# Optimization experiments

Hardware: AMD Instinct MI355X
Metric: run time of the kernel (lower is better)

The kernel has to match this reference:

```python
import jax, jax.numpy as jnp
import numpy as np

B, S, D_MODEL, N_HEADS, MAX_LEN = 2, 1024, 1024, 16, 1024
D_K = D_MODEL // N_HEADS


def setup_inputs() -> dict:
    key = jax.random.key(0)
    ks = jax.random.split(key, 8)
    w_std = 1.0 / np.sqrt(D_MODEL)  # ~ torch Linear default scale
    inp = {
        "query": jax.random.normal(ks[0], (B, S, D_MODEL), jnp.float32),
        "key": jax.random.normal(ks[1], (B, S, D_MODEL), jnp.float32),
        "value": jax.random.normal(ks[2], (B, S, D_MODEL), jnp.float32),
        "Wq": jax.random.normal(ks[3], (D_MODEL, D_MODEL), jnp.float32) * w_std,
        "Wk": jax.random.normal(ks[4], (D_MODEL, D_MODEL), jnp.float32) * w_std,
        "Wv": jax.random.normal(ks[5], (D_MODEL, D_MODEL), jnp.float32) * w_std,
        "Wo": jax.random.normal(ks[6], (D_MODEL, D_MODEL), jnp.float32) * w_std,
        "bq": jnp.zeros((D_MODEL,), jnp.float32),
        "bk": jnp.zeros((D_MODEL,), jnp.float32),
        "bv": jnp.zeros((D_MODEL,), jnp.float32),
        "bo": jnp.zeros((D_MODEL,), jnp.float32),
        "Er": jax.random.normal(ks[7], (2 * MAX_LEN - 1, D_K), jnp.float32) * 0.02,
    }
    return inp


def _rel_positions(q_len, k_len, max_len):
    pos = jnp.arange(q_len)[:, None] - jnp.arange(k_len)[None, :]
    pos = jnp.clip(pos, -max_len + 1, max_len - 1)
    return pos + max_len - 1  # [q_len, k_len] indices into Er


def reference(query, key, value, Wq, Wk, Wv, Wo, bq, bk, bv, bo, Er):
    b, q_len, d_model = query.shape
    k_len = key.shape[1]
    d_k = Er.shape[-1]
    h = d_model // d_k
    scale = 1.0 / np.sqrt(d_k)

    def proj(x, W, bias):  # torch Linear: x @ W.T + b, then split heads -> [b,h,s,d_k]
        y = x @ W.T + bias
        return y.reshape(b, -1, h, d_k).transpose(0, 2, 1, 3)

    q = proj(query, Wq, bq)
    k = proj(key, Wk, bk)
    v = proj(value, Wv, bv)

    positions = _rel_positions(q_len, k_len, MAX_LEN)  # [q,k]
    # QEr[b,h,q,k] = sum_d q[b,h,q,d] * Er[positions[q,k], d]
    # computed as a full contraction against Er then a gather on the relative axis
    qe_all = jnp.einsum('bhqd,rd->bhqr', q, Er)  # [b,h,q,2*max_len-1]
    qer = jnp.take_along_axis(qe_all, positions[None, None, :, :], axis=-1)  # [b,h,q,k]

    qk = jnp.einsum('bhqd,bhkd->bhqk', q, k)
    scores = (qk + qer) * scale
    p_attn = jax.nn.softmax(scores, axis=-1)  # dropout=0.0 (eval)
    out = jnp.einsum('bhqk,bhkd->bhqd', p_attn, v)

    out = out.transpose(0, 2, 1, 3).reshape(b, q_len, h * d_k)
    return out @ Wo.T + bo
```

## Files before the change

### kernel.cpp

```cpp
#include <hip/hip_runtime.h>
#include <hip/hip_bf16.h>
#include <cstdint>
#include <cstddef>

typedef __attribute__((ext_vector_type(8))) short bf16x8;
typedef __attribute__((ext_vector_type(4))) float f32x4;
typedef unsigned short u16;
typedef unsigned int u32;

#define DEV static __device__ __forceinline__

constexpr int Sc = 1024, DMc = 1024, Hc = 16, DKc = 64;

DEV u16 f2bf(float f) {
  u32 u = __float_as_uint(f);
  return (u16)((u + 0x7FFFu + ((u >> 16) & 1u)) >> 16);
}
DEV float bf2f(u16 h) { return __uint_as_float(((u32)h) << 16); }

#define GLDS16(g, l)                                                        \
  __builtin_amdgcn_global_load_lds(                                         \
      (const __attribute__((address_space(1))) void*)(g),                   \
      (__attribute__((address_space(3))) void*)(l), 16, 0, 0)

struct CvtJob { const float* in; u16* out; int nchunk; int rsh; int nreal; };
struct CvtArgs { CvtJob j[8]; };

__global__ __launch_bounds__(256) void cvt_kernel(CvtArgs a) {
  CvtJob job = a.j[blockIdx.y];
  int ci = (int)(blockIdx.x * 256 + threadIdx.x);
  if (ci >= job.nchunk) return;
  bf16x8 o = {};
  if (ci < job.nreal) {
    const float* src = job.in + (size_t)ci * 8;
    float4 v0 = *(const float4*)src;
    float4 v1 = *(const float4*)(src + 4);
    o[0] = (short)f2bf(v0.x); o[1] = (short)f2bf(v0.y);
    o[2] = (short)f2bf(v0.z); o[3] = (short)f2bf(v0.w);
    o[4] = (short)f2bf(v1.x); o[5] = (short)f2bf(v1.y);
    o[6] = (short)f2bf(v1.z); o[7] = (short)f2bf(v1.w);
  }
  int row = ci >> job.rsh;
  int co = (ci & ~7) | ((ci & 7) ^ (row & 7));
  *(bf16x8*)(job.out + (size_t)co * 8) = o;
}

struct GemmJob { const u16* A; const u16* W; const float* bias; void* out; const float* aux; };
struct GemmArgs { GemmJob p[3]; };

template<int BM, int BN, int MODE>
__global__ __launch_bounds__(256, 2) void gemm_bt(GemmArgs G) {
  constexpr int MI = BM / 32, NI = BN / 32;
  __shared__ __align__(16) u16 sA[2][BM * 64];
  __shared__ __align__(16) u16 sB[2][BN * 64];
  const int tid = threadIdx.x, lane = tid & 63, w = tid >> 6;
  const int cl = lane & 15, rg = lane >> 4;
  const int srow = lane >> 3, schk = lane & 7;
  int z, m0, n0;
  if (MODE == 0) {
    int id = blockIdx.x;
    if (id < 512) {
      z = id >> 8;
      int r = id & 255, xcd = r & 7, t = r >> 3;
      m0 = (xcd * 4 + (t & 3)) * 64;
      n0 = (t >> 2) * 128;
    } else {
      z = 2;
      int r = id - 512, xcd = r & 7, t = r >> 3;
      n0 = (xcd * 2 + (t & 1)) * 128;
      m0 = (t >> 1) * 64;
    }
  } else {
    z = 0;
    int id = blockIdx.x, xcd = id & 7, t = id >> 3;
    m0 = (xcd * 4 + (t & 3)) * 64;
    n0 = (t >> 2) * 64;
  }
  GemmJob P = G.p[z];
  constexpr int K = 1024;
  const int wm = (w >> 1) * (BM / 2), wn = (w & 1) * (BN / 2);
  f32x4 acc[MI][NI] = {};

  bf16x8 ma[2][2];
  float  ml[2][2];

  auto stage = [&](int kt, int b) {
    if (MODE == 0) {
      const u16* Ab = P.A + (size_t)m0 * K + kt * 64;
      #pragma unroll
      for (int i = 0; i < BM / 32; ++i)
        GLDS16(Ab + (size_t)(i * 32 + w * 8 + srow) * K + schk * 8, &sA[b][(i * 32 + w * 8) * 64]);
    } else {
      #pragma unroll
      for (int i = 0; i < 2; ++i) {
        int ch = i * 256 + tid, row = ch >> 3, c = ch & 7;
        int rgl = m0 + row, bb = rgl >> 10, s = rgl & 1023;
        const u16* o0 = P.A + ((size_t)(bb * 16 + kt) * 1024 + s) * 64 + c * 8;
        ma[i][0] = *(const bf16x8*)o0;
        ma[i][1] = *(const bf16x8*)(o0 + (size_t)32 * 1024 * 64);
        ml[i][0] = P.aux[(size_t)(bb * 16 + kt) * 1024 + s];
        ml[i][1] = P.aux[(size_t)(32 + bb * 16 + kt) * 1024 + s];
      }
    }
    const u16* Wb = P.W + (size_t)n0 * K + kt * 64;
    #pragma unroll
    for (int i = 0; i < BN / 32; ++i)
      GLDS16(Wb + (size_t)(i * 32 + w * 8 + srow) * K + schk * 8, &sB[b][(i * 32 + w * 8) * 64]);
  };

  auto commit = [&](int b) {
    #pragma unroll
    for (int i = 0; i < 2; ++i) {
      int ch = i * 256 + tid, row = ch >> 3, c = ch & 7;
      float rinv = 1.0f / (ml[i][0] + ml[i][1]);
      bf16x8 v8;
      #pragma unroll
      for (int e = 0; e < 8; ++e)
        v8[e] = (short)f2bf((bf2f((u16)ma[i][0][e]) + bf2f((u16)ma[i][1][e])) * rinv);
      *(bf16x8*)(sA[b] + row * 64 + (c ^ (row & 7)) * 8) = v8;
    }
  };

  stage(0, 0);
  if (MODE == 1) commit(0);
  for (int kt = 0; kt < 16; ++kt) {
    __syncthreads();
    const int b = kt & 1;
    if (kt < 15) stage(kt + 1, b ^ 1);
    const u16* A_ = sA[b];
    const u16* B_ = sB[b];
    #pragma unroll
    for (int kk = 0; kk < 2; ++kk) {
      bf16x8 af[MI], bfr[NI];
      #pragma unroll
      for (int mi = 0; mi < MI; ++mi) {
        int row = wm + mi * 16 + cl;
        af[mi] = *(const bf16x8*)(A_ + row * 64 + ((kk * 4 + rg) ^ (row & 7)) * 8);
      }
      #pragma unroll
      for (int ni = 0; ni < NI; ++ni) {
        int row = wn + ni * 16 + cl;
        bfr[ni] = *(const bf16x8*)(B_ + row * 64 + ((kk * 4 + rg) ^ (row & 7)) * 8);
      }
      #pragma unroll
      for (int mi = 0; mi < MI; ++mi)
        #pragma unroll
        for (int ni = 0; ni < NI; ++ni)
          acc[mi][ni] = __builtin_amdgcn_mfma_f32_16x16x32_bf16(af[mi], bfr[ni], acc[mi][ni], 0, 0, 0);
    }
    if (MODE == 1 && kt < 15) commit(b ^ 1);
  }
  #pragma unroll
  for (int mi = 0; mi < MI; ++mi) {
    #pragma unroll
    for (int ni = 0; ni < NI; ++ni) {
      #pragma unroll
      for (int j = 0; j < 4; ++j) {
        int m = m0 + wm + mi * 16 + rg * 4 + j;
        int n = n0 + wn + ni * 16 + cl;
        if (MODE == 1) {
          ((float*)P.out)[(size_t)m * DMc + n] = acc[mi][ni][j] + P.bias[n];
        } else if (z < 2) {
          float v = acc[mi][ni][j] + P.bias[n];
          int h = n >> 6, d = n & 63;
          int c2 = (d >> 3) ^ (m & 7);
          ((u16*)P.out)[((size_t)((m >> 10) * Hc + h) * Sc + (m & 1023)) * DKc + c2 * 8 + (d & 7)] = f2bf(v);
        } else {
          float v = acc[mi][ni][j] + P.bias[m];
          int d = m & 63, h = m >> 6, bb = n >> 10, s = n & 1023;
          int c2 = ((s & 63) >> 3) ^ (d & 7);
          ((u16*)P.out)[((size_t)(bb * Hc + h) * DKc + d) * Sc + (s & ~63) + c2 * 8 + (s & 7)] = f2bf(v);
        }
      }
    }
  }
}

__global__ __launch_bounds__(256, 4) void attn_rel(
    const u16* __restrict__ qg, const u16* __restrict__ kg,
    const u16* __restrict__ vtg, const u16* __restrict__ erg,
    u16* __restrict__ Opart, float* __restrict__ lpart) {
  __shared__ __align__(16) u16 sK[64 * 64];
  __shared__ __align__(16) u16 sV[64 * 64];
  __shared__ __align__(16) u16 sU[4][1440];
  const int tid = threadIdx.x, lane = tid & 63, w = tid >> 6;
  const int cl = lane & 15, rg = lane >> 4;
  const int key = cl & 7;
  const int bh = blockIdx.x & 31, qt = (blockIdx.x >> 5) & 15, half = blockIdx.x >> 9;
  const int q0 = qt * 64, t0 = half * 8;

  const u16* qrow = qg + ((size_t)bh * Sc + q0 + w * 16 + cl) * DKc;
  bf16x8 qf0 = *(const bf16x8*)(qrow + (rg ^ key) * 8);
  bf16x8 qf1 = *(const bf16x8*)(qrow + ((rg + 4) ^ key) * 8);
  f32x4 oacc[4] = {};
  float lsum = 0.f;
  u16* Uw = sU[w];
  const u16* kbase = kg + (size_t)bh * Sc * DKc;
  const u16* vbase = vtg + (size_t)bh * DKc * Sc;

  auto stage = [&](int t) {
    const u16* ks = kbase + t * 64 * 64;
    #pragma unroll
    for (int i = 0; i < 2; ++i) {
      GLDS16(ks + (i * 32 + w * 8) * 64 + lane * 8, &sK[(i * 32 + w * 8) * 64]);
      GLDS16(vbase + (size_t)(i * 32 + w * 8 + (lane >> 3)) * Sc + t * 64 + (lane & 7) * 8,
             &sV[(i * 32 + w * 8) * 64]);
    }
  };

  stage(t0);
  for (int tt = 0; tt < 8; ++tt) {
    const int t = t0 + tt;
    __syncthreads();

    f32x4 sct[4];
    #pragma unroll
    for (int nc = 0; nc < 4; ++nc) {
      const u16* kr = sK + (nc * 16 + cl) * 64;
      bf16x8 b0 = *(const bf16x8*)(kr + (rg ^ key) * 8);
      bf16x8 b1 = *(const bf16x8*)(kr + ((rg + 4) ^ key) * 8);
      f32x4 a = {};
      a = __builtin_amdgcn_mfma_f32_16x16x32_bf16(b0, qf0, a, 0, 0, 0);
      a = __builtin_amdgcn_mfma_f32_16x16x32_bf16(b1, qf1, a, 0, 0, 0);
      sct[nc] = a;
    }
    const u16* ebase = erg + (size_t)(q0 + w * 16 - t * 64 + 960) * DKc;
    #pragma unroll
    for (int rc0 = 0; rc0 < 5; ++rc0) {
      const u16* er = ebase + (size_t)(rc0 * 16 + cl) * DKc;
      bf16x8 e0 = *(const bf16x8*)(er + (rg ^ key) * 8);
      bf16x8 e1 = *(const bf16x8*)(er + ((rg + 4) ^ key) * 8);
      f32x4 a = {};
      a = __builtin_amdgcn_mfma_f32_16x16x32_bf16(qf0, e0, a, 0, 0, 0);
      a = __builtin_amdgcn_mfma_f32_16x16x32_bf16(qf1, e1, a, 0, 0, 0);
      u16* tp = Uw + (rc0 * 16 + cl) * 18 + rg * 4;
      ushort2 lo, hi;
      lo.x = f2bf(a[0]); lo.y = f2bf(a[1]);
      hi.x = f2bf(a[2]); hi.y = f2bf(a[3]);
      *(ushort2*)tp = lo;
      *(ushort2*)(tp + 2) = hi;
    }
    float pv[4][4];
    #pragma unroll
    for (int nc = 0; nc < 4; ++nc) {
      #pragma unroll
      for (int j = 0; j < 4; ++j) {
        int r = cl + 63 - (nc * 16 + rg * 4 + j);
        float tval = bf2f(Uw[r * 18 + cl]);
        float p = __expf((sct[nc][j] + tval) * 0.125f);
        lsum += p;
        pv[nc][j] = p;
      }
    }
    #pragma unroll
    for (int nc = 0; nc < 4; ++nc) {
      ushort4 pk;
      pk.x = f2bf(pv[nc][0]); pk.y = f2bf(pv[nc][1]);
      pk.z = f2bf(pv[nc][2]); pk.w = f2bf(pv[nc][3]);
      *(ushort4*)(Uw + cl * 76 + nc * 16 + rg * 4) = pk;
    }
    bf16x8 pa0 = *(const bf16x8*)(Uw + cl * 76 + rg * 8);
    bf16x8 pa1 = *(const bf16x8*)(Uw + cl * 76 + 32 + rg * 8);
    #pragma unroll
    for (int dc = 0; dc < 4; ++dc) {
      const u16* vr = sV + (dc * 16 + cl) * 64;
      bf16x8 b0 = *(const bf16x8*)(vr + (rg ^ key) * 8);
      bf16x8 b1 = *(const bf16x8*)(vr + ((rg + 4) ^ key) * 8);
      oacc[dc] = __builtin_amdgcn_mfma_f32_16x16x32_bf16(pa0, b0, oacc[dc], 0, 0, 0);
      oacc[dc] = __builtin_amdgcn_mfma_f32_16x16x32_bf16(pa1, b1, oacc[dc], 0, 0, 0);
    }
    __syncthreads();
    if (tt < 7) stage(t + 1);
  }
  lsum += __shfl_xor(lsum, 16);
  lsum += __shfl_xor(lsum, 32);
  const size_t pb = (size_t)(half * 32 + bh) * Sc;
  if (rg == 0) lpart[pb + q0 + w * 16 + cl] = lsum;
  u16* Ob = Opart + (pb + q0 + w * 16) * DKc;
  #pragma unroll
  for (int dc = 0; dc < 4; ++dc)
    #pragma unroll
    for (int j = 0; j < 4; ++j)
      Ob[(rg * 4 + j) * DKc + dc * 16 + cl] = f2bf(oacc[dc][j]);
}

extern "C" void kernel_launch(void* const* d_in, const int* in_sizes, int n_in,
                              void* d_out, int out_size, void* d_ws, size_t ws_size,
                              hipStream_t stream) {
  (void)in_sizes; (void)n_in; (void)out_size; (void)ws_size;
  const float* query = (const float*)d_in[0];
  const float* key_  = (const float*)d_in[1];
  const float* value = (const float*)d_in[2];
  const float* Wq = (const float*)d_in[3];
  const float* Wk = (const float*)d_in[4];
  const float* Wv = (const float*)d_in[5];
  const float* Wo = (const float*)d_in[6];
  const float* bq = (const float*)d_in[7];
  const float* bk = (const float*)d_in[8];
  const float* bv = (const float*)d_in[9];
  const float* bo = (const float*)d_in[10];
  const float* Er = (const float*)d_in[11];

  char* p = (char*)d_ws;
  size_t off = 0;
  auto alloc = [&](size_t bytes) {
    char* r = p + off;
    off += (bytes + 255) & ~(size_t)255;
    return r;
  };
  u16* Xq  = (u16*)alloc((size_t)2048 * 1024 * 2);
  u16* Xk  = (u16*)alloc((size_t)2048 * 1024 * 2);
  u16* Xv  = (u16*)alloc((size_t)2048 * 1024 * 2);
  u16* Wqb = (u16*)alloc((size_t)1024 * 1024 * 2);
  u16* Wkb = (u16*)alloc((size_t)1024 * 1024 * 2);
  u16* Wvb = (u16*)alloc((size_t)1024 * 1024 * 2);
  u16* Wob = (u16*)alloc((size_t)1024 * 1024 * 2);
  u16* Erb = (u16*)alloc((size_t)2048 * 64 * 2);
  u16* qh  = (u16*)alloc((size_t)2048 * 1024 * 2);
  u16* kh  = (u16*)alloc((size_t)2048 * 1024 * 2);
  u16* vt  = (u16*)alloc((size_t)2048 * 1024 * 2);
  u16* Opart = (u16*)alloc((size_t)2 * 32 * 1024 * 64 * 2);
  float* lpart = (float*)alloc((size_t)2 * 32 * 1024 * 4);

  CvtArgs ca;
  ca.j[0] = {query, Xq, 262144, 7, 262144};
  ca.j[1] = {key_,  Xk, 262144, 7, 262144};
  ca.j[2] = {value, Xv, 262144, 7, 262144};
  ca.j[3] = {Wq, Wqb, 131072, 7, 131072};
  ca.j[4] = {Wk, Wkb, 131072, 7, 131072};
  ca.j[5] = {Wv, Wvb, 131072, 7, 131072};
  ca.j[6] = {Wo, Wob, 131072, 7, 131072};
  ca.j[7] = {Er, Erb, 16384, 3, 16376};
  cvt_kernel<<<dim3(1024, 8, 1), 256, 0, stream>>>(ca);

  GemmArgs gp;
  gp.p[0] = {Xq, Wqb, bq, (void*)qh, nullptr};
  gp.p[1] = {Xk, Wkb, bk, (void*)kh, nullptr};
  gp.p[2] = {Wvb, Xv, bv, (void*)vt, nullptr};
  gemm_bt<64, 128, 0><<<dim3(768, 1, 1), 256, 0, stream>>>(gp);

  attn_rel<<<dim3(1024, 1, 1), 256, 0, stream>>>(qh, kh, vt, Erb, Opart, lpart);

  GemmArgs go;
  go.p[0] = {Opart, Wob, bo, d_out, lpart};
  go.p[1] = go.p[0];
  go.p[2] = go.p[0];
  gemm_bt<64, 64, 1><<<dim3(512, 1, 1), 256, 0, stream>>>(go);
}
```

Baseline: 92.54 us.

## Give each attention wave two 16-row query subtiles to reuse K/V fragments

The attention kernel now runs 2 waves per block instead of 4, and each wave handles 32 query rows as two 16-row subtiles. K and V fragments loaded from LDS are reused across both subtiles, halving LDS reads per MFMA. It also adds s_setprio around the MFMA sections. The cost is higher register pressure from doubled accumulators and query fragments, fewer waves per block for latency hiding, and each thread issuing twice as many staging loads.

```diff
diff --git a/kernel.cpp b/kernel.cpp
--- a/kernel.cpp
+++ b/kernel.cpp
@@ -176,35 +176,38 @@
   }
 }
 
-__global__ __launch_bounds__(256, 4) void attn_rel(
+__global__ __launch_bounds__(128, 3) void attn_rel(
     const u16* __restrict__ qg, const u16* __restrict__ kg,
     const u16* __restrict__ vtg, const u16* __restrict__ erg,
     u16* __restrict__ Opart, float* __restrict__ lpart) {
   __shared__ __align__(16) u16 sK[64 * 64];
   __shared__ __align__(16) u16 sV[64 * 64];
-  __shared__ __align__(16) u16 sU[4][1440];
+  __shared__ __align__(16) u16 sU[2][2][1440];
   const int tid = threadIdx.x, lane = tid & 63, w = tid >> 6;
   const int cl = lane & 15, rg = lane >> 4;
   const int key = cl & 7;
   const int bh = blockIdx.x & 31, qt = (blockIdx.x >> 5) & 15, half = blockIdx.x >> 9;
   const int q0 = qt * 64, t0 = half * 8;
 
-  const u16* qrow = qg + ((size_t)bh * Sc + q0 + w * 16 + cl) * DKc;
-  bf16x8 qf0 = *(const bf16x8*)(qrow + (rg ^ key) * 8);
-  bf16x8 qf1 = *(const bf16x8*)(qrow + ((rg + 4) ^ key) * 8);
-  f32x4 oacc[4] = {};
-  float lsum = 0.f;
-  u16* Uw = sU[w];
+  bf16x8 qf[2][2];
+  #pragma unroll
+  for (int sub = 0; sub < 2; ++sub) {
+    const u16* qrow = qg + ((size_t)bh * Sc + q0 + w * 32 + sub * 16 + cl) * DKc;
+    qf[sub][0] = *(const bf16x8*)(qrow + (rg ^ key) * 8);
+    qf[sub][1] = *(const bf16x8*)(qrow + ((rg + 4) ^ key) * 8);
+  }
+  f32x4 oacc[2][4] = {};
+  float lsum[2] = {0.f, 0.f};
   const u16* kbase = kg + (size_t)bh * Sc * DKc;
   const u16* vbase = vtg + (size_t)bh * DKc * Sc;
 
   auto stage = [&](int t) {
     const u16* ks = kbase + t * 64 * 64;
     #pragma unroll
-    for (int i = 0; i < 2; ++i) {
-      GLDS16(ks + (i * 32 + w * 8) * 64 + lane * 8, &sK[(i * 32 + w * 8) * 64]);
-      GLDS16(vbase + (size_t)(i * 32 + w * 8 + (lane >> 3)) * Sc + t * 64 + (lane & 7) * 8,
-             &sV[(i * 32 + w * 8) * 64]);
+    for (int i = 0; i < 4; ++i) {
+      GLDS16(ks + (i * 16 + w * 8) * 64 + lane * 8, &sK[(i * 16 + w * 8) * 64]);
+      GLDS16(vbase + (size_t)(i * 16 + w * 8 + (lane >> 3)) * Sc + t * 64 + (lane & 7) * 8,
+             &sV[(i * 16 + w * 8) * 64]);
     }
   };
 
@@ -213,75 +216,102 @@
     const int t = t0 + tt;
     __syncthreads();
 
-    f32x4 sct[4];
+    f32x4 sct[2][4];
+    __builtin_amdgcn_s_setprio(1);
     #pragma unroll
     for (int nc = 0; nc < 4; ++nc) {
       const u16* kr = sK + (nc * 16 + cl) * 64;
       bf16x8 b0 = *(const bf16x8*)(kr + (rg ^ key) * 8);
       bf16x8 b1 = *(const bf16x8*)(kr + ((rg + 4) ^ key) * 8);
-      f32x4 a = {};
-      a = __builtin_amdgcn_mfma_f32_16x16x32_bf16(b0, qf0, a, 0, 0, 0);
-      a = __builtin_amdgcn_mfma_f32_16x16x32_bf16(b1, qf1, a, 0, 0, 0);
-      sct[nc] = a;
-    }
-    const u16* ebase = erg + (size_t)(q0 + w * 16 - t * 64 + 960) * DKc;
-    #pragma unroll
-    for (int rc0 = 0; rc0 < 5; ++rc0) {
-      const u16* er = ebase + (size_t)(rc0 * 16 + cl) * DKc;
-      bf16x8 e0 = *(const bf16x8*)(er + (rg ^ key) * 8);
-      bf16x8 e1 = *(const bf16x8*)(er + ((rg + 4) ^ key) * 8);
-      f32x4 a = {};
-      a = __builtin_amdgcn_mfma_f32_16x16x32_bf16(qf0, e0, a, 0, 0, 0);
-      a = __builtin_amdgcn_mfma_f32_16x16x32_bf16(qf1, e1, a, 0, 0, 0);
-      u16* tp = Uw + (rc0 * 16 + cl) * 18 + rg * 4;
-      ushort2 lo, hi;
-      lo.x = f2bf(a[0]); lo.y = f2bf(a[1]);
-      hi.x = f2bf(a[2]); hi.y = f2bf(a[3]);
-      *(ushort2*)tp = lo;
-      *(ushort2*)(tp + 2) = hi;
-    }
-    float pv[4][4];
-    #pragma unroll
-    for (int nc = 0; nc < 4; ++nc) {
-      #pragma unroll
-      for (int j = 0; j < 4; ++j) {
-        int r = cl + 63 - (nc * 16 + rg * 4 + j);
-        float tval = bf2f(Uw[r * 18 + cl]);
-        float p = __expf((sct[nc][j] + tval) * 0.125f);
-        lsum += p;
-        pv[nc][j] = p;
-      }
-    }
-    #pragma unroll
-    for (int nc = 0; nc < 4; ++nc) {
-      ushort4 pk;
-      pk.x = f2bf(pv[nc][0]); pk.y = f2bf(pv[nc][1]);
-      pk.z = f2bf(pv[nc][2]); pk.w = f2bf(pv[nc][3]);
-      *(ushort4*)(Uw + cl * 76 + nc * 16 + rg * 4) = pk;
-    }
-    bf16x8 pa0 = *(const bf16x8*)(Uw + cl * 76 + rg * 8);
-    bf16x8 pa1 = *(const bf16x8*)(Uw + cl * 76 + 32 + rg * 8);
+      #pragma unroll
+      for (int sub = 0; sub < 2; ++sub) {
+        f32x4 a = {};
+        a = __builtin_amdgcn_mfma_f32_16x16x32_bf16(b0, qf[sub][0], a, 0, 0, 0);
+        a = __builtin_amdgcn_mfma_f32_16x16x32_bf16(b1, qf[sub][1], a, 0, 0, 0);
+        sct[sub][nc] = a;
+      }
+    }
+    __builtin_amdgcn_s_setprio(0);
+
+    #pragma unroll
+    for (int sub = 0; sub < 2; ++sub) {
+      u16* Uw = sU[w][sub];
+      const u16* ebase = erg + (size_t)(q0 + w * 32 + sub * 16 - t * 64 + 960) * DKc;
+      #pragma unroll
+      for (int rc0 = 0; rc0 < 5; ++rc0) {
+        const u16* er = ebase + (size_t)(rc0 * 16 + cl) * DKc;
+        bf16x8 e0 = *(const bf16x8*)(er + (rg ^ key) * 8);
+        bf16x8 e1 = *(const bf16x8*)(er + ((rg + 4) ^ key) * 8);
+        f32x4 a = {};
+        a = __builtin_amdgcn_mfma_f32_16x16x32_bf16(qf[sub][0], e0, a, 0, 0, 0);
+        a = __builtin_amdgcn_mfma_f32_16x16x32_bf16(qf[sub][1], e1, a, 0, 0, 0);
+        u16* tp = Uw + (rc0 * 16 + cl) * 18 + rg * 4;
+        ushort2 lo, hi;
+        lo.x = f2bf(a[0]); lo.y = f2bf(a[1]);
+        hi.x = f2bf(a[2]); hi.y = f2bf(a[3]);
+        *(ushort2*)tp = lo;
+        *(ushort2*)(tp + 2) = hi;
+      }
+    }
+    #pragma unroll
+    for (int sub = 0; sub < 2; ++sub) {
+      u16* Uw = sU[w][sub];
+      float pv[4][4];
+      #pragma unroll
+      for (int nc = 0; nc < 4; ++nc) {
+        #pragma unroll
+        for (int j = 0; j < 4; ++j) {
+          int r = cl + 63 - (nc * 16 + rg * 4 + j);
+          float tval = bf2f(Uw[r * 18 + cl]);
+          float p = __expf((sct[sub][nc][j] + tval) * 0.125f);
+          lsum[sub] += p;
+          pv[nc][j] = p;
+        }
+      }
+      #pragma unroll
+      for (int nc = 0; nc < 4; ++nc) {
+        ushort4 pk;
+        pk.x = f2bf(pv[nc][0]); pk.y = f2bf(pv[nc][1]);
+        pk.z = f2bf(pv[nc][2]); pk.w = f2bf(pv[nc][3]);
+        *(ushort4*)(Uw + cl * 76 + nc * 16 + rg * 4) = pk;
+      }
+    }
+    bf16x8 pa[2][2];
+    #pragma unroll
+    for (int sub = 0; sub < 2; ++sub) {
+      pa[sub][0] = *(const bf16x8*)(sU[w][sub] + cl * 76 + rg * 8);
+      pa[sub][1] = *(const bf16x8*)(sU[w][sub] + cl * 76 + 32 + rg * 8);
+    }
+    __builtin_amdgcn_s_setprio(1);
     #pragma unroll
     for (int dc = 0; dc < 4; ++dc) {
       const u16* vr = sV + (dc * 16 + cl) * 64;
       bf16x8 b0 = *(const bf16x8*)(vr + (rg ^ key) * 8);
       bf16x8 b1 = *(const bf16x8*)(vr + ((rg + 4) ^ key) * 8);
-      oacc[dc] = __builtin_amdgcn_mfma_f32_16x16x32_bf16(pa0, b0, oacc[dc], 0, 0, 0);
-      oacc[dc] = __builtin_amdgcn_mfma_f32_16x16x32_bf16(pa1, b1, oacc[dc], 0, 0, 0);
-    }
+      #pragma unroll
+      for (int sub = 0; sub < 2; ++sub) {
+        oacc[sub][dc] = __builtin_amdgcn_mfma_f32_16x16x32_bf16(pa[sub][0], b0, oacc[sub][dc], 0, 0, 0);
+        oacc[sub][dc] = __builtin_amdgcn_mfma_f32_16x16x32_bf16(pa[sub][1], b1, oacc[sub][dc], 0, 0, 0);
+      }
+    }
+    __builtin_amdgcn_s_setprio(0);
     __syncthreads();
     if (tt < 7) stage(t + 1);
   }
-  lsum += __shfl_xor(lsum, 16);
-  lsum += __shfl_xor(lsum, 32);
   const size_t pb = (size_t)(half * 32 + bh) * Sc;
-  if (rg == 0) lpart[pb + q0 + w * 16 + cl] = lsum;
-  u16* Ob = Opart + (pb + q0 + w * 16) * DKc;
   #pragma unroll
-  for (int dc = 0; dc < 4; ++dc)
-    #pragma unroll
-    for (int j = 0; j < 4; ++j)
-      Ob[(rg * 4 + j) * DKc + dc * 16 + cl] = f2bf(oacc[dc][j]);
+  for (int sub = 0; sub < 2; ++sub) {
+    float l = lsum[sub];
+    l += __shfl_xor(l, 16);
+    l += __shfl_xor(l, 32);
+    if (rg == 0) lpart[pb + q0 + w * 32 + sub * 16 + cl] = l;
+    u16* Ob = Opart + (pb + q0 + w * 32 + sub * 16) * DKc;
+    #pragma unroll
+    for (int dc = 0; dc < 4; ++dc)
+      #pragma unroll
+      for (int j = 0; j < 4; ++j)
+        Ob[(rg * 4 + j) * DKc + dc * 16 + cl] = f2bf(oacc[sub][dc][j]);
+  }
 }
 
 extern "C" void kernel_launch(void* const* d_in, const int* in_sizes, int n_in,
@@ -339,7 +369,7 @@
   gp.p[2] = {Wvb, Xv, bv, (void*)vt, nullptr};
   gemm_bt<64, 128, 0><<<dim3(768, 1, 1), 256, 0, stream>>>(gp);
 
-  attn_rel<<<dim3(1024, 1, 1), 256, 0, stream>>>(qh, kh, vt, Erb, Opart, lpart);
+  attn_rel<<<dim3(1024, 1, 1), 128, 0, stream>>>(qh, kh, vt, Erb, Opart, lpart);
 
   GemmArgs go;
   go.p[0] = {Opart, Wob, bo, d_out, lpart};
```

Result: slower. 102.4 us (+10.7%).

## Fuse fp32-to-bf16 conversion of query/key into projection GEMM A-tile loads

Applied to the files above, without the earlier changes.

The separate conversion pass for the query and key activations is removed. The Q/K projection GEMM now loads fp32 rows straight into registers, converts them to bf16 and writes them swizzled into LDS, using a two-stage register prefetch with an unrolled-by-two k loop. This removes a full write and re-read of two 4 MB bf16 buffers plus part of the convert launch. In exchange the A-operand path now does register-staged loads and in-kernel conversion, which adds register pressure and VALU work inside the GEMM's main loop. The GEMM template is also split into separate projection and output kernels.

```diff
diff --git a/kernel.cpp b/kernel.cpp
--- a/kernel.cpp
+++ b/kernel.cpp
@@ -24,7 +24,7 @@
       (__attribute__((address_space(3))) void*)(l), 16, 0, 0)
 
 struct CvtJob { const float* in; u16* out; int nchunk; int rsh; int nreal; };
-struct CvtArgs { CvtJob j[8]; };
+struct CvtArgs { CvtJob j[6]; };
 
 __global__ __launch_bounds__(256) void cvt_kernel(CvtArgs a) {
   CvtJob job = a.j[blockIdx.y];
@@ -45,69 +45,163 @@
   *(bf16x8*)(job.out + (size_t)co * 8) = o;
 }
 
-struct GemmJob { const u16* A; const u16* W; const float* bias; void* out; const float* aux; };
-struct GemmArgs { GemmJob p[3]; };
-
-template<int BM, int BN, int MODE>
-__global__ __launch_bounds__(256, 2) void gemm_bt(GemmArgs G) {
-  constexpr int MI = BM / 32, NI = BN / 32;
-  __shared__ __align__(16) u16 sA[2][BM * 64];
-  __shared__ __align__(16) u16 sB[2][BN * 64];
+struct ProjJob { const u16* A; const u16* W; const float* bias; u16* out; const float* Xf; };
+struct ProjArgs { ProjJob p[3]; };
+
+__global__ __launch_bounds__(256, 2) void gemm_proj(ProjArgs G) {
+  __shared__ __align__(16) u16 sA[2][64 * 64];
+  __shared__ __align__(16) u16 sB[2][128 * 64];
   const int tid = threadIdx.x, lane = tid & 63, w = tid >> 6;
   const int cl = lane & 15, rg = lane >> 4;
   const int srow = lane >> 3, schk = lane & 7;
   int z, m0, n0;
-  if (MODE == 0) {
-    int id = blockIdx.x;
-    if (id < 512) {
-      z = id >> 8;
-      int r = id & 255, xcd = r & 7, t = r >> 3;
-      m0 = (xcd * 4 + (t & 3)) * 64;
-      n0 = (t >> 2) * 128;
-    } else {
-      z = 2;
-      int r = id - 512, xcd = r & 7, t = r >> 3;
-      n0 = (xcd * 2 + (t & 1)) * 128;
-      m0 = (t >> 1) * 64;
-    }
+  int id = blockIdx.x;
+  if (id < 512) {
+    z = id >> 8;
+    int r = id & 255, xcd = r & 7, t = r >> 3;
+    m0 = (xcd * 4 + (t & 3)) * 64;
+    n0 = (t >> 2) * 128;
   } else {
-    z = 0;
-    int id = blockIdx.x, xcd = id & 7, t = id >> 3;
-    m0 = (xcd * 4 + (t & 3)) * 64;
-    n0 = (t >> 2) * 64;
-  }
-  GemmJob P = G.p[z];
+    z = 2;
+    int r = id - 512, xcd = r & 7, t = r >> 3;
+    n0 = (xcd * 2 + (t & 1)) * 128;
+    m0 = (t >> 1) * 64;
+  }
+  ProjJob P = G.p[z];
   constexpr int K = 1024;
-  const int wm = (w >> 1) * (BM / 2), wn = (w & 1) * (BN / 2);
-  f32x4 acc[MI][NI] = {};
-
+  const int wm = (w >> 1) * 32, wn = (w & 1) * 64;
+  f32x4 acc[2][4] = {};
+  float4 fA[2][2], fB[2][2];
+
+  auto issueX = [&](int kt, float4 (*dst)[2]) {
+    #pragma unroll
+    for (int i = 0; i < 2; ++i) {
+      int ch = i * 256 + tid, row = ch >> 3, c = ch & 7;
+      const float* src = P.Xf + (size_t)(m0 + row) * K + kt * 64 + c * 8;
+      dst[i][0] = *(const float4*)src;
+      dst[i][1] = *(const float4*)(src + 4);
+    }
+  };
+  auto commitX = [&](const float4 (*rs)[2], int b) {
+    #pragma unroll
+    for (int i = 0; i < 2; ++i) {
+      int ch = i * 256 + tid, row = ch >> 3, c = ch & 7;
+      const float* f = (const float*)&rs[i][0];
+      bf16x8 v8;
+      #pragma unroll
+      for (int e = 0; e < 8; ++e) v8[e] = (short)f2bf(f[e]);
+      *(bf16x8*)(sA[b] + row * 64 + (c ^ (row & 7)) * 8) = v8;
+    }
+  };
+  auto stageA = [&](int kt, int b) {
+    const u16* Ab = P.A + (size_t)m0 * K + kt * 64;
+    #pragma unroll
+    for (int i = 0; i < 2; ++i)
+      GLDS16(Ab + (size_t)(i * 32 + w * 8 + srow) * K + schk * 8, &sA[b][(i * 32 + w * 8) * 64]);
+  };
+  auto stageB = [&](int kt, int b) {
+    const u16* Wb = P.W + (size_t)n0 * K + kt * 64;
+    #pragma unroll
+    for (int i = 0; i < 4; ++i)
+      GLDS16(Wb + (size_t)(i * 32 + w * 8 + srow) * K + schk * 8, &sB[b][(i * 32 + w * 8) * 64]);
+  };
+  auto mfma_step = [&](int b) {
+    #pragma unroll
+    for (int kk = 0; kk < 2; ++kk) {
+      bf16x8 af[2], bfr[4];
+      #pragma unroll
+      for (int mi = 0; mi < 2; ++mi) {
+        int row = wm + mi * 16 + cl;
+        af[mi] = *(const bf16x8*)(sA[b] + row * 64 + ((kk * 4 + rg) ^ (row & 7)) * 8);
+      }
+      #pragma unroll
+      for (int ni = 0; ni < 4; ++ni) {
+        int row = wn + ni * 16 + cl;
+        bfr[ni] = *(const bf16x8*)(sB[b] + row * 64 + ((kk * 4 + rg) ^ (row & 7)) * 8);
+      }
+      #pragma unroll
+      for (int mi = 0; mi < 2; ++mi)
+        #pragma unroll
+        for (int ni = 0; ni < 4; ++ni)
+          acc[mi][ni] = __builtin_amdgcn_mfma_f32_16x16x32_bf16(af[mi], bfr[ni], acc[mi][ni], 0, 0, 0);
+    }
+  };
+
+  const bool inl = (z < 2);
+  if (inl) { issueX(0, fA); issueX(1, fB); commitX(fA, 0); }
+  else stageA(0, 0);
+  stageB(0, 0);
+  for (int kt2 = 0; kt2 < 16; kt2 += 2) {
+    __syncthreads();
+    if (inl) { if (kt2 + 2 < 16) issueX(kt2 + 2, fA); }
+    else if (kt2 + 1 < 16) stageA(kt2 + 1, 1);
+    if (kt2 + 1 < 16) stageB(kt2 + 1, 1);
+    mfma_step(0);
+    if (inl) commitX(fB, 1);
+    __syncthreads();
+    if (inl) { if (kt2 + 3 < 16) issueX(kt2 + 3, fB); }
+    else if (kt2 + 2 < 16) stageA(kt2 + 2, 0);
+    if (kt2 + 2 < 16) stageB(kt2 + 2, 0);
+    mfma_step(1);
+    if (inl && kt2 + 2 < 16) commitX(fA, 0);
+  }
+  #pragma unroll
+  for (int mi = 0; mi < 2; ++mi) {
+    #pragma unroll
+    for (int ni = 0; ni < 4; ++ni) {
+      #pragma unroll
+      for (int j = 0; j < 4; ++j) {
+        int m = m0 + wm + mi * 16 + rg * 4 + j;
+        int n = n0 + wn + ni * 16 + cl;
+        if (z < 2) {
+          float v = acc[mi][ni][j] + P.bias[n];
+          int h = n >> 6, d = n & 63;
+          int c2 = (d >> 3) ^ (m & 7);
+          P.out[((size_t)((m >> 10) * Hc + h) * Sc + (m & 1023)) * DKc + c2 * 8 + (d & 7)] = f2bf(v);
+        } else {
+          float v = acc[mi][ni][j] + P.bias[m];
+          int d = m & 63, h = m >> 6, bb = n >> 10, s = n & 1023;
+          int c2 = ((s & 63) >> 3) ^ (d & 7);
+          P.out[((size_t)(bb * Hc + h) * DKc + d) * Sc + (s & ~63) + c2 * 8 + (s & 7)] = f2bf(v);
+        }
+      }
+    }
+  }
+}
+
+struct OutArgs { const u16* O; const u16* W; const float* bias; float* out; const float* l; };
+
+__global__ __launch_bounds__(256, 2) void gemm_out(OutArgs P) {
+  __shared__ __align__(16) u16 sA[2][64 * 64];
+  __shared__ __align__(16) u16 sB[2][64 * 64];
+  const int tid = threadIdx.x, lane = tid & 63, w = tid >> 6;
+  const int cl = lane & 15, rg = lane >> 4;
+  const int srow = lane >> 3, schk = lane & 7;
+  int id = blockIdx.x, xcd = id & 7, t = id >> 3;
+  const int m0 = (xcd * 4 + (t & 3)) * 64;
+  const int n0 = (t >> 2) * 64;
+  constexpr int K = 1024;
+  const int wm = (w >> 1) * 32, wn = (w & 1) * 32;
+  f32x4 acc[2][2] = {};
   bf16x8 ma[2][2];
   float  ml[2][2];
 
   auto stage = [&](int kt, int b) {
-    if (MODE == 0) {
-      const u16* Ab = P.A + (size_t)m0 * K + kt * 64;
-      #pragma unroll
-      for (int i = 0; i < BM / 32; ++i)
-        GLDS16(Ab + (size_t)(i * 32 + w * 8 + srow) * K + schk * 8, &sA[b][(i * 32 + w * 8) * 64]);
-    } else {
-      #pragma unroll
-      for (int i = 0; i < 2; ++i) {
-        int ch = i * 256 + tid, row = ch >> 3, c = ch & 7;
-        int rgl = m0 + row, bb = rgl >> 10, s = rgl & 1023;
-        const u16* o0 = P.A + ((size_t)(bb * 16 + kt) * 1024 + s) * 64 + c * 8;
-        ma[i][0] = *(const bf16x8*)o0;
-        ma[i][1] = *(const bf16x8*)(o0 + (size_t)32 * 1024 * 64);
-        ml[i][0] = P.aux[(size_t)(bb * 16 + kt) * 1024 + s];
-        ml[i][1] = P.aux[(size_t)(32 + bb * 16 + kt) * 1024 + s];
-      }
+    #pragma unroll
+    for (int i = 0; i < 2; ++i) {
+      int ch = i * 256 + tid, row = ch >> 3, c = ch & 7;
+      int rgl = m0 + row, bb = rgl >> 10, s = rgl & 1023;
+      const u16* o0 = P.O + ((size_t)(bb * 16 + kt) * 1024 + s) * 64 + c * 8;
+      ma[i][0] = *(const bf16x8*)o0;
+      ma[i][1] = *(const bf16x8*)(o0 + (size_t)32 * 1024 * 64);
+      ml[i][0] = P.l[(size_t)(bb * 16 + kt) * 1024 + s];
+      ml[i][1] = P.l[(size_t)(32 + bb * 16 + kt) * 1024 + s];
     }
     const u16* Wb = P.W + (size_t)n0 * K + kt * 64;
     #pragma unroll
-    for (int i = 0; i < BN / 32; ++i)
+    for (int i = 0; i < 2; ++i)
       GLDS16(Wb + (size_t)(i * 32 + w * 8 + srow) * K + schk * 8, &sB[b][(i * 32 + w * 8) * 64]);
   };
-
   auto commit = [&](int b) {
     #pragma unroll
     for (int i = 0; i < 2; ++i) {
@@ -122,58 +216,42 @@
   };
 
   stage(0, 0);
-  if (MODE == 1) commit(0);
+  commit(0);
   for (int kt = 0; kt < 16; ++kt) {
     __syncthreads();
     const int b = kt & 1;
     if (kt < 15) stage(kt + 1, b ^ 1);
-    const u16* A_ = sA[b];
-    const u16* B_ = sB[b];
     #pragma unroll
     for (int kk = 0; kk < 2; ++kk) {
-      bf16x8 af[MI], bfr[NI];
-      #pragma unroll
-      for (int mi = 0; mi < MI; ++mi) {
+      bf16x8 af[2], bfr[2];
+      #pragma unroll
+      for (int mi = 0; mi < 2; ++mi) {
         int row = wm + mi * 16 + cl;
-        af[mi] = *(const bf16x8*)(A_ + row * 64 + ((kk * 4 + rg) ^ (row & 7)) * 8);
-      }
-      #pragma unroll
-      for (int ni = 0; ni < NI; ++ni) {
+        af[mi] = *(const bf16x8*)(sA[b] + row * 64 + ((kk * 4 + rg) ^ (row & 7)) * 8);
+      }
+      #pragma unroll
+      for (int ni = 0; ni < 2; ++ni) {
         int row = wn + ni * 16 + cl;
-        bfr[ni] = *(const bf16x8*)(B_ + row * 64 + ((kk * 4 + rg) ^ (row & 7)) * 8);
-      }
-      #pragma unroll
-      for (int mi = 0; mi < MI; ++mi)
+        bfr[ni] = *(const bf16x8*)(sB[b] + row * 64 + ((kk * 4 + rg) ^ (row & 7)) * 8);
+      }
+      #pragma unroll
+      for (int mi = 0; mi < 2; ++mi)
         #pragma unroll
-        for (int ni = 0; ni < NI; ++ni)
+        for (int ni = 0; ni < 2; ++ni)
           acc[mi][ni] = __builtin_amdgcn_mfma_f32_16x16x32_bf16(af[mi], bfr[ni], acc[mi][ni], 0, 0, 0);
     }
-    if (MODE == 1 && kt < 15) commit(b ^ 1);
+    if (kt < 15) commit(b ^ 1);
   }
   #pragma unroll
-  for (int mi = 0; mi < MI; ++mi) {
-    #pragma unroll
-    for (int ni = 0; ni < NI; ++ni) {
+  for (int mi = 0; mi < 2; ++mi)
+    #pragma unroll
+    for (int ni = 0; ni < 2; ++ni)
       #pragma unroll
       for (int j = 0; j < 4; ++j) {
         int m = m0 + wm + mi * 16 + rg * 4 + j;
         int n = n0 + wn + ni * 16 + cl;
-        if (MODE == 1) {
-          ((float*)P.out)[(size_t)m * DMc + n] = acc[mi][ni][j] + P.bias[n];
-        } else if (z < 2) {
-          float v = acc[mi][ni][j] + P.bias[n];
-          int h = n >> 6, d = n & 63;
-          int c2 = (d >> 3) ^ (m & 7);
-          ((u16*)P.out)[((size_t)((m >> 10) * Hc + h) * Sc + (m & 1023)) * DKc + c2 * 8 + (d & 7)] = f2bf(v);
-        } else {
-          float v = acc[mi][ni][j] + P.bias[m];
-          int d = m & 63, h = m >> 6, bb = n >> 10, s = n & 1023;
-          int c2 = ((s & 63) >> 3) ^ (d & 7);
-          ((u16*)P.out)[((size_t)(bb * Hc + h) * DKc + d) * Sc + (s & ~63) + c2 * 8 + (s & 7)] = f2bf(v);
-        }
-      }
-    }
-  }
+        P.out[(size_t)m * DMc + n] = acc[mi][ni][j] + P.bias[n];
+      }
 }
 
 __global__ __launch_bounds__(256, 4) void attn_rel(
@@ -308,8 +386,6 @@
     off += (bytes + 255) & ~(size_t)255;
     return r;
   };
-  u16* Xq  = (u16*)alloc((size_t)2048 * 1024 * 2);
-  u16* Xk  = (u16*)alloc((size_t)2048 * 1024 * 2);
   u16* Xv  = (u16*)alloc((size_t)2048 * 1024 * 2);
   u16* Wqb = (u16*)alloc((size_t)1024 * 1024 * 2);
   u16* Wkb = (u16*)alloc((size_t)1024 * 1024 * 2);
@@ -323,27 +399,22 @@
   float* lpart = (float*)alloc((size_t)2 * 32 * 1024 * 4);
 
   CvtArgs ca;
-  ca.j[0] = {query, Xq, 262144, 7, 262144};
-  ca.j[1] = {key_,  Xk, 262144, 7, 262144};
-  ca.j[2] = {value, Xv, 262144, 7, 262144};
-  ca.j[3] = {Wq, Wqb, 131072, 7, 131072};
-  ca.j[4] = {Wk, Wkb, 131072, 7, 131072};
-  ca.j[5] = {Wv, Wvb, 131072, 7, 131072};
-  ca.j[6] = {Wo, Wob, 131072, 7, 131072};
-  ca.j[7] = {Er, Erb, 16384, 3, 16376};
-  cvt_kernel<<<dim3(1024, 8, 1), 256, 0, stream>>>(ca);
-
-  GemmArgs gp;
-  gp.p[0] = {Xq, Wqb, bq, (void*)qh, nullptr};
-  gp.p[1] = {Xk, Wkb, bk, (void*)kh, nullptr};
-  gp.p[2] = {Wvb, Xv, bv, (void*)vt, nullptr};
-  gemm_bt<64, 128, 0><<<dim3(768, 1, 1), 256, 0, stream>>>(gp);
+  ca.j[0] = {value, Xv, 262144, 7, 262144};
+  ca.j[1] = {Wq, Wqb, 131072, 7, 131072};
+  ca.j[2] = {Wk, Wkb, 131072, 7, 131072};
+  ca.j[3] = {Wv, Wvb, 131072, 7, 131072};
+  ca.j[4] = {Wo, Wob, 131072, 7, 131072};
+  ca.j[5] = {Er, Erb, 16384, 3, 16376};
+  cvt_kernel<<<dim3(1024, 6, 1), 256, 0, stream>>>(ca);
+
+  ProjArgs pr;
+  pr.p[0] = {nullptr, Wqb, bq, qh, query};
+  pr.p[1] = {nullptr, Wkb, bk, kh, key_};
+  pr.p[2] = {Wvb, Xv, bv, vt, nullptr};
+  gemm_proj<<<dim3(768, 1, 1), 256, 0, stream>>>(pr);
 
   attn_rel<<<dim3(1024, 1, 1), 256, 0, stream>>>(qh, kh, vt, Erb, Opart, lpart);
 
-  GemmArgs go;
-  go.p[0] = {Opart, Wob, bo, d_out, lpart};
-  go.p[1] = go.p[0];
-  go.p[2] = go.p[0];
-  gemm_bt<64, 64, 1><<<dim3(512, 1, 1), 256, 0, stream>>>(go);
-}
+  OutArgs go = {Opart, Wob, bo, (float*)d_out, lpart};
+  gemm_out<<<dim3(512, 1, 1), 256, 0, stream>>>(go);
+}
```

Measured after the change: 95.08 us. +2.7%, slower.
